# Kernel tuning notes

Hardware: AMD Instinct MI355X
Metric: run time of the kernel (lower is better)

The kernel has to match this reference:

```python
import jax, jax.numpy as jnp
import numpy as np

N = 20000
E = 320000
NEG_SLOPE = 0.2
LN_EPS = 1e-5


def gat_conv(x, W, a_src, a_dst, b, src, dst, heads, ch, concat):
    # x: [N, F_in]; W: [F_in, H*C]; a_src/a_dst: [H, C]; b: [H*C] or [C]
    xl = (x @ W).reshape(N, heads, ch)                      # [N,H,C]
    alpha_src = jnp.sum(xl * a_src, axis=-1)                # [N,H]
    alpha_dst = jnp.sum(xl * a_dst, axis=-1)                # [N,H]
    e = alpha_src[src] + alpha_dst[dst]                     # [E',H]
    e = jax.nn.leaky_relu(e, NEG_SLOPE)
    # segment softmax over incoming edges of each dst node
    m = jax.ops.segment_max(e, dst, num_segments=N)         # [N,H]
    m = jnp.where(jnp.isfinite(m), m, 0.0)
    ex = jnp.exp(e - m[dst])
    denom = jax.ops.segment_sum(ex, dst, num_segments=N)    # [N,H]
    alpha = ex / (denom[dst] + 1e-16)                       # [E',H]
    msg = alpha[:, :, None] * xl[src]                       # [E',H,C]
    out = jax.ops.segment_sum(msg, dst, num_segments=N)     # [N,H,C]
    if concat:
        return out.reshape(N, heads * ch) + b
    return out.mean(axis=1) + b


def layer_norm(x, g, b):
    mu = jnp.mean(x, axis=-1, keepdims=True)
    var = jnp.mean(jnp.square(x - mu), axis=-1, keepdims=True)
    return (x - mu) * jax.lax.rsqrt(var + LN_EPS) * g + b


def setup_inputs() -> dict:
    key = jax.random.key(0)
    ks = jax.random.split(key, 24)
    d = {}
    d["x"] = jax.random.normal(ks[0], (N, 50), dtype=jnp.float32)
    d["edge_index"] = jax.random.randint(ks[1], (2, E), 0, N, dtype=jnp.int64)

    def glorot(k, shape):
        fan = shape[0] + shape[-1]
        return jax.random.normal(k, shape, dtype=jnp.float32) * np.sqrt(2.0 / fan)

    # conv1: 50 -> 256, heads=4, concat
    d["W1"] = glorot(ks[2], (50, 4 * 256))
    d["a_src1"] = glorot(ks[3], (4, 256))
    d["a_dst1"] = glorot(ks[4], (4, 256))
    d["b1"] = jnp.zeros((4 * 256,), jnp.float32)
    # conv2: 1024 -> 256, heads=4, concat
    d["W2"] = glorot(ks[5], (1024, 4 * 256))
    d["a_src2"] = glorot(ks[6], (4, 256))
    d["a_dst2"] = glorot(ks[7], (4, 256))
    d["b2"] = jnp.zeros((4 * 256,), jnp.float32)
    # conv3: 1024 -> 121, heads=6, concat=False
    d["W3"] = glorot(ks[8], (1024, 6 * 121))
    d["a_src3"] = glorot(ks[9], (6, 121))
    d["a_dst3"] = glorot(ks[10], (6, 121))
    d["b3"] = jnp.zeros((121,), jnp.float32)
    # skips
    d["skipW1"] = glorot(ks[11], (50, 1024))
    d["skipb1"] = jnp.zeros((1024,), jnp.float32)
    d["skipW2"] = glorot(ks[12], (1024, 1024))
    d["skipb2"] = jnp.zeros((1024,), jnp.float32)
    # layer norms
    d["g1"] = jnp.ones((1024,), jnp.float32)
    d["beta1"] = jnp.zeros((1024,), jnp.float32)
    d["g2"] = jnp.ones((1024,), jnp.float32)
    d["beta2"] = jnp.zeros((1024,), jnp.float32)
    return d


def reference(x, edge_index, W1, a_src1, a_dst1, b1, W2, a_src2, a_dst2, b2,
              W3, a_src3, a_dst3, b3, skipW1, skipb1, skipW2, skipb2,
              g1, beta1, g2, beta2):
    # add self loops (PyG GATConv default)
    loop = jnp.arange(N, dtype=edge_index.dtype)
    src = jnp.concatenate([edge_index[0], loop])
    dst = jnp.concatenate([edge_index[1], loop])

    h = gat_conv(x, W1, a_src1, a_dst1, b1, src, dst, 4, 256, True)
    h = jax.nn.elu(layer_norm(h + (x @ skipW1 + skipb1), g1, beta1))
    h2 = gat_conv(h, W2, a_src2, a_dst2, b2, src, dst, 4, 256, True)
    h2 = jax.nn.elu(layer_norm(h2 + (h @ skipW2 + skipb2), g2, beta2))
    out = gat_conv(h2, W3, a_src3, a_dst3, b3, src, dst, 6, 121, False)
    return out
```

## Files before the change

kernel.cpp:

```cpp
#include <hip/hip_runtime.h>
#include <hip/hip_bf16.h>
#include <math.h>

typedef __attribute__((ext_vector_type(8))) __bf16 bf16x8;
typedef __attribute__((ext_vector_type(4))) float f32x4;

#if __has_builtin(__builtin_amdgcn_global_load_lds)
#define HAVE_GLD 1
#define GLD16(g, l)                                                                      \
    __builtin_amdgcn_global_load_lds(                                                    \
        (const __attribute__((address_space(1))) unsigned int*)(g),                      \
        (__attribute__((address_space(3))) unsigned int*)(l), 16, 0, 0)
#else
#define HAVE_GLD 0
#endif

__global__ __launch_bounds__(256) void gemm_bt(const __bf16* __restrict__ A,
                                               const __bf16* __restrict__ Bt,
                                               __bf16* __restrict__ C,
                                               int M, int N, int K) {
    __shared__ __bf16 As[128 * 32];
    __shared__ __bf16 Bs[128 * 32];
    const int t = threadIdx.x;
    const int lane = t & 63;
    const int wid = t >> 6;
    const int wm = (wid >> 1) << 6;
    const int wn = (wid & 1) << 6;
    const int bm = blockIdx.x * 128;
    const int bn = blockIdx.y * 128;

    const int srow = (wid << 4) + (lane >> 2);
    const int scol = (lane & 3) << 3;

    f32x4 acc[4][4];
#pragma unroll
    for (int i = 0; i < 4; i++)
#pragma unroll
        for (int j = 0; j < 4; j++) acc[i][j] = (f32x4){0.f, 0.f, 0.f, 0.f};

    const int m16 = lane & 15;
    const int k8 = (lane >> 4) << 3;

    for (int k0 = 0; k0 < K; k0 += 32) {
        __syncthreads();
#if HAVE_GLD
        GLD16(A + (size_t)(bm + srow) * K + k0 + scol, As + srow * 32 + scol);
        GLD16(A + (size_t)(bm + 64 + srow) * K + k0 + scol, As + (64 + srow) * 32 + scol);
        GLD16(Bt + (size_t)(bn + srow) * K + k0 + scol, Bs + srow * 32 + scol);
        GLD16(Bt + (size_t)(bn + 64 + srow) * K + k0 + scol, Bs + (64 + srow) * 32 + scol);
#else
        {
            bf16x8 a0 = *(const bf16x8*)(A + (size_t)(bm + srow) * K + k0 + scol);
            bf16x8 a1 = *(const bf16x8*)(A + (size_t)(bm + 64 + srow) * K + k0 + scol);
            bf16x8 b0 = *(const bf16x8*)(Bt + (size_t)(bn + srow) * K + k0 + scol);
            bf16x8 b1 = *(const bf16x8*)(Bt + (size_t)(bn + 64 + srow) * K + k0 + scol);
            *(bf16x8*)(As + srow * 32 + scol) = a0;
            *(bf16x8*)(As + (64 + srow) * 32 + scol) = a1;
            *(bf16x8*)(Bs + srow * 32 + scol) = b0;
            *(bf16x8*)(Bs + (64 + srow) * 32 + scol) = b1;
        }
#endif
        __syncthreads();
        bf16x8 af[4], bfr[4];
#pragma unroll
        for (int i = 0; i < 4; i++) {
            af[i] = *(const bf16x8*)(As + (wm + 16 * i + m16) * 32 + k8);
            bfr[i] = *(const bf16x8*)(Bs + (wn + 16 * i + m16) * 32 + k8);
        }
#pragma unroll
        for (int i = 0; i < 4; i++)
#pragma unroll
            for (int j = 0; j < 4; j++)
                acc[i][j] = __builtin_amdgcn_mfma_f32_16x16x32_bf16(af[i], bfr[j], acc[i][j], 0, 0, 0);
    }
    const int r4 = (lane >> 4) << 2;
#pragma unroll
    for (int i = 0; i < 4; i++) {
#pragma unroll
        for (int j = 0; j < 4; j++) {
            int col = bn + wn + 16 * j + m16;
#pragma unroll
            for (int r = 0; r < 4; r++) {
                int row = bm + wm + 16 * i + r4 + r;
                C[(size_t)row * N + col] = (__bf16)acc[i][j][r];
            }
        }
    }
}

__global__ void pack_x_k(const float* __restrict__ x, __bf16* __restrict__ xp, int rows_real) {
    int i = blockIdx.x * 256 + threadIdx.x;
    int n = i >> 6, c = i & 63;
    float v = 0.f;
    if (n < rows_real && c < 50) v = x[n * 50 + c];
    xp[(size_t)n * 64 + c] = (__bf16)v;
}

__global__ void transpose_pad_k(const float* __restrict__ W, __bf16* __restrict__ WT,
                                int K, int N, int Kp, int Np) {
    __shared__ float tile[32][33];
    int bx = blockIdx.x, by = blockIdx.y;
    int tx = threadIdx.x & 31, ty = threadIdx.x >> 5;
#pragma unroll
    for (int r = ty; r < 32; r += 8) {
        int k = by * 32 + r, n = bx * 32 + tx;
        float v = 0.f;
        if (k < K && n < N) v = W[(size_t)k * N + n];
        tile[r][tx] = v;
    }
    __syncthreads();
#pragma unroll
    for (int r = ty; r < 32; r += 8) {
        int n = bx * 32 + r, k = by * 32 + tx;
        if (n < Np && k < Kp) WT[(size_t)n * Kp + k] = (__bf16)tile[tx][r];
    }
}

__global__ void transpose_pad_w3_k(const float* __restrict__ W, __bf16* __restrict__ WT) {
    __shared__ float tile[32][33];
    int bx = blockIdx.x, by = blockIdx.y;
    int tx = threadIdx.x & 31, ty = threadIdx.x >> 5;
    int r0 = bx * 32;
    int h = r0 >> 7;
    int c0 = r0 & 127;
#pragma unroll
    for (int r = ty; r < 32; r += 8) {
        int k = by * 32 + r;
        int c = c0 + tx;
        float v = 0.f;
        if (c < 121) v = W[(size_t)k * 726 + h * 121 + c];
        tile[r][tx] = v;
    }
    __syncthreads();
#pragma unroll
    for (int r = ty; r < 32; r += 8) {
        int rr = r0 + r;
        int k = by * 32 + tx;
        WT[(size_t)rr * 1024 + k] = (__bf16)tile[tx][r];
    }
}

__global__ void probe_ei_k(const int* __restrict__ ei, int* __restrict__ flag) {
    if (blockIdx.x == 0 && threadIdx.x == 0) {
        int all0 = 1;
        for (int i = 0; i < 64; i++)
            if (ei[2 * i + 1] != 0) { all0 = 0; break; }
        *flag = all0;
    }
}

__device__ __forceinline__ int load_ei(const int* ei, int idx, int is64) {
    return is64 ? ei[2 * idx] : ei[idx];
}

__global__ void hist_k(const int* __restrict__ ei, const int* __restrict__ flag,
                       int* __restrict__ cnt, int E, int Nn) {
    int e = blockIdx.x * 256 + threadIdx.x;
    if (e >= E + Nn) return;
    int is64 = *flag;
    int d = (e < E) ? load_ei(ei, E + e, is64) : (e - E);
    d = min(max(d, 0), Nn - 1);
    atomicAdd(&cnt[d], 1);
}

__global__ __launch_bounds__(1024) void scan_k(const int* __restrict__ cnt, int* __restrict__ row_ptr,
                                               int Nn, int total) {
    __shared__ int part[1024];
    int t = threadIdx.x;
    int chunk = (Nn + 1023) >> 10;
    int lo = t * chunk;
    int hi = lo + chunk; if (hi > Nn) hi = Nn; if (lo > Nn) lo = Nn;
    int s = 0;
    for (int i = lo; i < hi; i++) s += cnt[i];
    part[t] = s;
    __syncthreads();
    for (int off = 1; off < 1024; off <<= 1) {
        int v = (t >= off) ? part[t - off] : 0;
        __syncthreads();
        part[t] += v;
        __syncthreads();
    }
    int run = part[t] - s;
    for (int i = lo; i < hi; i++) { row_ptr[i] = run; run += cnt[i]; }
    if (t == 0) row_ptr[Nn] = total;
}

__global__ void fill_csr_k(const int* __restrict__ ei, const int* __restrict__ flag,
                           const int* __restrict__ row_ptr, int* __restrict__ cursor,
                           int* __restrict__ src_csr, int E, int Nn) {
    int e = blockIdx.x * 256 + threadIdx.x;
    if (e >= E + Nn) return;
    int is64 = *flag;
    int d = (e < E) ? load_ei(ei, E + e, is64) : (e - E);
    int s = (e < E) ? load_ei(ei, e, is64) : (e - E);
    d = min(max(d, 0), Nn - 1);
    s = min(max(s, 0), Nn - 1);
    int slot = row_ptr[d] + atomicAdd(&cursor[d], 1);
    src_csr[slot] = s;
}

__global__ void alpha_k(const __bf16* __restrict__ XL, int ld, const float* __restrict__ a_src,
                        const float* __restrict__ a_dst, float* __restrict__ asrc,
                        float* __restrict__ adst, int Nn, int H, int C, int Cpad) {
    int gw = (blockIdx.x * 256 + threadIdx.x) >> 6;
    int lane = threadIdx.x & 63;
    if (gw >= Nn * H) return;
    int n = gw / H, h = gw - n * H;
    const __bf16* row = XL + (size_t)n * ld + h * Cpad;
    const float* as = a_src + h * C;
    const float* ad = a_dst + h * C;
    float s = 0.f, d = 0.f;
    for (int c = lane; c < C; c += 64) {
        float v = (float)row[c];
        s += v * as[c];
        d += v * ad[c];
    }
#pragma unroll
    for (int off = 32; off; off >>= 1) {
        s += __shfl_down(s, off);
        d += __shfl_down(d, off);
    }
    if (lane == 0) { asrc[n * H + h] = s; adst[n * H + h] = d; }
}

__global__ void attn_k(const int* __restrict__ row_ptr, const int* __restrict__ src_csr,
                       const float* __restrict__ asrc, const float* __restrict__ adst,
                       float* __restrict__ w, int Nn, int H) {
    int gw = (blockIdx.x * 256 + threadIdx.x) >> 6;
    int lane = threadIdx.x & 63;
    if (gw >= Nn) return;
    int n = gw;
    int base = row_ptr[n], deg = row_ptr[n + 1] - base;
    for (int h = 0; h < H; h++) {
        float ad = adst[n * H + h];
        float m = -1e30f;
        for (int s = lane; s < deg; s += 64) {
            float e = asrc[src_csr[base + s] * H + h] + ad;
            e = e > 0.f ? e : 0.2f * e;
            m = fmaxf(m, e);
        }
#pragma unroll
        for (int off = 1; off < 64; off <<= 1) m = fmaxf(m, __shfl_xor(m, off));
        float sum = 0.f;
        for (int s = lane; s < deg; s += 64) {
            float e = asrc[src_csr[base + s] * H + h] + ad;
            e = e > 0.f ? e : 0.2f * e;
            sum += __expf(e - m);
        }
#pragma unroll
        for (int off = 1; off < 64; off <<= 1) sum += __shfl_xor(sum, off);
        float inv = 1.f / (sum + 1e-16f);
        for (int s = lane; s < deg; s += 64) {
            float e = asrc[src_csr[base + s] * H + h] + ad;
            e = e > 0.f ? e : 0.2f * e;
            w[(size_t)(base + s) * H + h] = __expf(e - m) * inv;
        }
    }
}

__global__ __launch_bounds__(256) void agg_skip5(const __bf16* __restrict__ XL,
                                                 const float* __restrict__ w,
                                                 const int* __restrict__ row_ptr,
                                                 const int* __restrict__ src_csr,
                                                 const float* __restrict__ bias,
                                                 const float* __restrict__ sb,
                                                 __bf16* __restrict__ SK, int Nn) {
    const int cc = blockIdx.x;
    const int n = blockIdx.y * 4 + (threadIdx.x >> 6);
    const int lane = threadIdx.x & 63;
    if (n >= Nn) return;
    const int g = lane >> 4;
    const int p = lane & 15;
    const int col = cc * 128 + p * 8;
    const int head = cc >> 1;
    const int base = row_ptr[n], end = row_ptr[n + 1];

    float acc[8];
#pragma unroll
    for (int j = 0; j < 8; j++) acc[j] = 0.f;

    for (int e = base; e < end; e += 16) {
        int sidx[4];
        float wv[4];
#pragma unroll
        for (int s = 0; s < 4; s++) {
            int idx = e + g + 4 * s;
            bool v = idx < end;
            sidx[s] = v ? src_csr[idx] : src_csr[base];
            wv[s] = v ? w[(size_t)idx * 4 + head] : 0.f;
        }
#pragma unroll
        for (int s = 0; s < 4; s++) {
            bf16x8 xv = *(const bf16x8*)(XL + (size_t)sidx[s] * 1024 + col);
#pragma unroll
            for (int j = 0; j < 8; j++) acc[j] += wv[s] * (float)xv[j];
        }
    }
#pragma unroll
    for (int j = 0; j < 8; j++) {
        acc[j] += __shfl_xor(acc[j], 16);
        acc[j] += __shfl_xor(acc[j], 32);
    }
    if (lane < 16) {
        size_t o = (size_t)n * 1024 + col;
        bf16x8 sk = *(const bf16x8*)(SK + o);
        bf16x8 res;
#pragma unroll
        for (int j = 0; j < 8; j++)
            res[j] = (__bf16)(acc[j] + bias[col + j] + sb[col + j] + (float)sk[j]);
        *(bf16x8*)(SK + o) = res;
    }
}

__global__ __launch_bounds__(256) void agg_mean5(const __bf16* __restrict__ XL,
                                                 const float* __restrict__ w,
                                                 const int* __restrict__ row_ptr,
                                                 const int* __restrict__ src_csr,
                                                 __bf16* __restrict__ part, int Nn) {
    const int cc = blockIdx.x;
    const int n = blockIdx.y * 4 + (threadIdx.x >> 6);
    const int lane = threadIdx.x & 63;
    if (n >= Nn) return;
    const int g = lane >> 4;
    const int p = lane & 15;
    const int col = cc * 128 + p * 8;
    const int base = row_ptr[n], end = row_ptr[n + 1];

    float acc[8];
#pragma unroll
    for (int j = 0; j < 8; j++) acc[j] = 0.f;

    for (int e = base; e < end; e += 16) {
        int sidx[4];
        float wv[4];
#pragma unroll
        for (int s = 0; s < 4; s++) {
            int idx = e + g + 4 * s;
            bool v = idx < end;
            sidx[s] = v ? src_csr[idx] : src_csr[base];
            wv[s] = v ? w[(size_t)idx * 6 + cc] : 0.f;
        }
#pragma unroll
        for (int s = 0; s < 4; s++) {
            bf16x8 xv = *(const bf16x8*)(XL + (size_t)sidx[s] * 768 + col);
#pragma unroll
            for (int j = 0; j < 8; j++) acc[j] += wv[s] * (float)xv[j];
        }
    }
#pragma unroll
    for (int j = 0; j < 8; j++) {
        acc[j] += __shfl_xor(acc[j], 16);
        acc[j] += __shfl_xor(acc[j], 32);
    }
    if (lane < 16) {
        size_t o = (size_t)n * 768 + col;
        bf16x8 res;
#pragma unroll
        for (int j = 0; j < 8; j++) res[j] = (__bf16)acc[j];
        *(bf16x8*)(part + o) = res;
    }
}

__global__ __launch_bounds__(128) void reduce_mean_k(const __bf16* __restrict__ part,
                                                     const float* __restrict__ b3,
                                                     float* __restrict__ out, int Nn) {
    int n = blockIdx.x;
    int t = threadIdx.x;
    if (t >= 121) return;
    const __bf16* row = part + (size_t)n * 768;
    float s = 0.f;
#pragma unroll
    for (int h = 0; h < 6; h++) s += (float)row[h * 128 + t];
    out[(size_t)n * 121 + t] = s * (1.f / 6.f) + b3[t];
}

__global__ __launch_bounds__(256) void ln_elu_k(const __bf16* __restrict__ in,
                                                const float* __restrict__ g,
                                                const float* __restrict__ be,
                                                __bf16* __restrict__ out, int rows_real) {
    const int D = 1024;
    int n = blockIdx.x;
    int t = threadIdx.x;
    size_t ro = (size_t)n * D;
    if (n >= rows_real) {
#pragma unroll
        for (int j = 0; j < 4; j++) out[ro + t + 256 * j] = (__bf16)0.f;
        return;
    }
    float v[4];
    float s = 0.f, q = 0.f;
#pragma unroll
    for (int j = 0; j < 4; j++) {
        int c = t + 256 * j;
        float a = (float)in[ro + c];
        v[j] = a;
        s += a;
        q += a * a;
    }
#pragma unroll
    for (int off = 32; off; off >>= 1) {
        s += __shfl_down(s, off);
        q += __shfl_down(q, off);
    }
    __shared__ float rs[8];
    int wid = t >> 6;
    if ((t & 63) == 0) { rs[wid] = s; rs[wid + 4] = q; }
    __syncthreads();
    s = rs[0] + rs[1] + rs[2] + rs[3];
    q = rs[4] + rs[5] + rs[6] + rs[7];
    float mu = s * (1.f / 1024.f);
    float var = q * (1.f / 1024.f) - mu * mu;
    float inv = rsqrtf(fmaxf(var, 0.f) + 1e-5f);
#pragma unroll
    for (int j = 0; j < 4; j++) {
        int c = t + 256 * j;
        float y = (v[j] - mu) * inv * g[c] + be[c];
        y = y > 0.f ? y : expm1f(y);
        out[ro + c] = (__bf16)y;
    }
}

extern "C" void kernel_launch(void* const* d_in, const int* in_sizes, int n_in,
                              void* d_out, int out_size, void* d_ws, size_t ws_size,
                              hipStream_t stream) {
    const float* x   = (const float*)d_in[0];
    const int*   ei  = (const int*)d_in[1];
    const float* W1  = (const float*)d_in[2];
    const float* as1 = (const float*)d_in[3];
    const float* ad1 = (const float*)d_in[4];
    const float* b1  = (const float*)d_in[5];
    const float* W2  = (const float*)d_in[6];
    const float* as2 = (const float*)d_in[7];
    const float* ad2 = (const float*)d_in[8];
    const float* b2  = (const float*)d_in[9];
    const float* W3  = (const float*)d_in[10];
    const float* as3 = (const float*)d_in[11];
    const float* ad3 = (const float*)d_in[12];
    const float* b3  = (const float*)d_in[13];
    const float* sW1 = (const float*)d_in[14];
    const float* sb1 = (const float*)d_in[15];
    const float* sW2 = (const float*)d_in[16];
    const float* sb2 = (const float*)d_in[17];
    const float* g1  = (const float*)d_in[18];
    const float* be1 = (const float*)d_in[19];
    const float* g2  = (const float*)d_in[20];
    const float* be2 = (const float*)d_in[21];
    float* out = (float*)d_out;

    const int Nn = 20000;
    const int E = in_sizes[1] / 2;
    const int E2 = E + Nn;
    const int Mpad = 20096;

    char* p = (char*)d_ws;
    auto alloc = [&](size_t bytes) {
        char* r = p;
        p += (bytes + 255) & ~(size_t)255;
        return r;
    };
    __bf16* W1pT  = (__bf16*)alloc((size_t)1024 * 64 * 2);
    __bf16* sW1T  = (__bf16*)alloc((size_t)1024 * 64 * 2);
    __bf16* W2T   = (__bf16*)alloc((size_t)1024 * 1024 * 2);
    __bf16* sW2T  = (__bf16*)alloc((size_t)1024 * 1024 * 2);
    __bf16* W3pT  = (__bf16*)alloc((size_t)768 * 1024 * 2);
    __bf16* xp    = (__bf16*)alloc((size_t)Mpad * 64 * 2);
    __bf16* XL    = (__bf16*)alloc((size_t)Mpad * 1024 * 2);
    __bf16* SK    = (__bf16*)alloc((size_t)Mpad * 1024 * 2);
    __bf16* H1    = (__bf16*)alloc((size_t)Mpad * 1024 * 2);
    float*  asrcb = (float*)alloc((size_t)Nn * 6 * 4);
    float*  adstb = (float*)alloc((size_t)Nn * 6 * 4);
    float*  wbuf  = (float*)alloc((size_t)E2 * 6 * 4);
    int*    rowp  = (int*)alloc((size_t)(Nn + 1) * 4);
    int*    cnt   = (int*)alloc((size_t)Nn * 4);
    int*    scsr  = (int*)alloc((size_t)E2 * 4);
    int*    eiflag= (int*)alloc(256);
    __bf16* part  = SK;
    (void)ws_size; (void)n_in; (void)out_size;

    pack_x_k<<<(Mpad * 64) / 256, 256, 0, stream>>>(x, xp, Nn);
    transpose_pad_k<<<dim3(32, 2), 256, 0, stream>>>(W1, W1pT, 50, 1024, 64, 1024);
    transpose_pad_k<<<dim3(32, 2), 256, 0, stream>>>(sW1, sW1T, 50, 1024, 64, 1024);
    transpose_pad_k<<<dim3(32, 32), 256, 0, stream>>>(W2, W2T, 1024, 1024, 1024, 1024);
    transpose_pad_k<<<dim3(32, 32), 256, 0, stream>>>(sW2, sW2T, 1024, 1024, 1024, 1024);
    transpose_pad_w3_k<<<dim3(24, 32), 256, 0, stream>>>(W3, W3pT);

    probe_ei_k<<<1, 64, 0, stream>>>(ei, eiflag);
    hipMemsetAsync(cnt, 0, (size_t)Nn * 4, stream);
    hist_k<<<(E2 + 255) / 256, 256, 0, stream>>>(ei, eiflag, cnt, E, Nn);
    scan_k<<<1, 1024, 0, stream>>>(cnt, rowp, Nn, E2);
    hipMemsetAsync(cnt, 0, (size_t)Nn * 4, stream);
    fill_csr_k<<<(E2 + 255) / 256, 256, 0, stream>>>(ei, eiflag, rowp, cnt, scsr, E, Nn);

    gemm_bt<<<dim3(Mpad / 128, 8), 256, 0, stream>>>(xp, W1pT, XL, Mpad, 1024, 64);
    gemm_bt<<<dim3(Mpad / 128, 8), 256, 0, stream>>>(xp, sW1T, SK, Mpad, 1024, 64);
    alpha_k<<<(Nn * 4 * 64) / 256, 256, 0, stream>>>(XL, 1024, as1, ad1, asrcb, adstb, Nn, 4, 256, 256);
    attn_k<<<(Nn + 3) / 4, 256, 0, stream>>>(rowp, scsr, asrcb, adstb, wbuf, Nn, 4);
    agg_skip5<<<dim3(8, (Nn + 3) / 4), 256, 0, stream>>>(XL, wbuf, rowp, scsr, b1, sb1, SK, Nn);
    ln_elu_k<<<Mpad, 256, 0, stream>>>(SK, g1, be1, H1, Nn);

    gemm_bt<<<dim3(Mpad / 128, 8), 256, 0, stream>>>(H1, W2T, XL, Mpad, 1024, 1024);
    gemm_bt<<<dim3(Mpad / 128, 8), 256, 0, stream>>>(H1, sW2T, SK, Mpad, 1024, 1024);
    alpha_k<<<(Nn * 4 * 64) / 256, 256, 0, stream>>>(XL, 1024, as2, ad2, asrcb, adstb, Nn, 4, 256, 256);
    attn_k<<<(Nn + 3) / 4, 256, 0, stream>>>(rowp, scsr, asrcb, adstb, wbuf, Nn, 4);
    agg_skip5<<<dim3(8, (Nn + 3) / 4), 256, 0, stream>>>(XL, wbuf, rowp, scsr, b2, sb2, SK, Nn);
    ln_elu_k<<<Mpad, 256, 0, stream>>>(SK, g2, be2, H1, Nn);

    gemm_bt<<<dim3(Mpad / 128, 6), 256, 0, stream>>>(H1, W3pT, XL, Mpad, 768, 1024);
    alpha_k<<<(Nn * 6 * 64) / 256, 256, 0, stream>>>(XL, 768, as3, ad3, asrcb, adstb, Nn, 6, 121, 128);
    attn_k<<<(Nn + 3) / 4, 256, 0, stream>>>(rowp, scsr, asrcb, adstb, wbuf, Nn, 6);
    agg_mean5<<<dim3(6, (Nn + 3) / 4), 256, 0, stream>>>(XL, wbuf, rowp, scsr, part, Nn);
    reduce_mean_k<<<Nn, 128, 0, stream>>>(part, b3, out, Nn);
}
```

Before: 851.2 us.

## Pad CSR rows to 16 and store attention weights head-major for vector loads

Each node's CSR segment is rounded up to a multiple of 16 and zero-filled, and attention weights are stored as separate per-head planes. The aggregation kernels can then load source indices and weights as 16-byte vectors without bounds checks or the strided per-head weight gather. The cost is extra memsets of the enlarged CSR and weight buffers, padded zero-weight edges that still gather row 0 of XL, and a separate degree array (the fill cursor) to keep the true counts.

```diff
diff --git a/kernel.cpp b/kernel.cpp
--- a/kernel.cpp
+++ b/kernel.cpp
@@ -4,6 +4,7 @@
 
 typedef __attribute__((ext_vector_type(8))) __bf16 bf16x8;
 typedef __attribute__((ext_vector_type(4))) float f32x4;
+typedef __attribute__((ext_vector_type(4))) int i32x4;
 
 #if __has_builtin(__builtin_amdgcn_global_load_lds)
 #define HAVE_GLD 1
@@ -164,14 +165,14 @@
 }
 
 __global__ __launch_bounds__(1024) void scan_k(const int* __restrict__ cnt, int* __restrict__ row_ptr,
-                                               int Nn, int total) {
+                                               int Nn) {
     __shared__ int part[1024];
     int t = threadIdx.x;
     int chunk = (Nn + 1023) >> 10;
     int lo = t * chunk;
     int hi = lo + chunk; if (hi > Nn) hi = Nn; if (lo > Nn) lo = Nn;
     int s = 0;
-    for (int i = lo; i < hi; i++) s += cnt[i];
+    for (int i = lo; i < hi; i++) s += (cnt[i] + 15) & ~15;
     part[t] = s;
     __syncthreads();
     for (int off = 1; off < 1024; off <<= 1) {
@@ -181,8 +182,8 @@
         __syncthreads();
     }
     int run = part[t] - s;
-    for (int i = lo; i < hi; i++) { row_ptr[i] = run; run += cnt[i]; }
-    if (t == 0) row_ptr[Nn] = total;
+    for (int i = lo; i < hi; i++) { row_ptr[i] = run; run += (cnt[i] + 15) & ~15; }
+    if (t == 1023) row_ptr[Nn] = part[1023];
 }
 
 __global__ void fill_csr_k(const int* __restrict__ ei, const int* __restrict__ flag,
@@ -223,18 +224,19 @@
     if (lane == 0) { asrc[n * H + h] = s; adst[n * H + h] = d; }
 }
 
-__global__ void attn_k(const int* __restrict__ row_ptr, const int* __restrict__ src_csr,
+__global__ void attn_k(const int* __restrict__ row_ptr, const int* __restrict__ deg,
+                       const int* __restrict__ src_csr,
                        const float* __restrict__ asrc, const float* __restrict__ adst,
-                       float* __restrict__ w, int Nn, int H) {
+                       float* __restrict__ wt, int Nn, int H, int Epad) {
     int gw = (blockIdx.x * 256 + threadIdx.x) >> 6;
     int lane = threadIdx.x & 63;
     if (gw >= Nn) return;
     int n = gw;
-    int base = row_ptr[n], deg = row_ptr[n + 1] - base;
+    int base = row_ptr[n], dg = deg[n];
     for (int h = 0; h < H; h++) {
         float ad = adst[n * H + h];
         float m = -1e30f;
-        for (int s = lane; s < deg; s += 64) {
+        for (int s = lane; s < dg; s += 64) {
             float e = asrc[src_csr[base + s] * H + h] + ad;
             e = e > 0.f ? e : 0.2f * e;
             m = fmaxf(m, e);
@@ -242,7 +244,7 @@
 #pragma unroll
         for (int off = 1; off < 64; off <<= 1) m = fmaxf(m, __shfl_xor(m, off));
         float sum = 0.f;
-        for (int s = lane; s < deg; s += 64) {
+        for (int s = lane; s < dg; s += 64) {
             float e = asrc[src_csr[base + s] * H + h] + ad;
             e = e > 0.f ? e : 0.2f * e;
             sum += __expf(e - m);
@@ -250,21 +252,22 @@
 #pragma unroll
         for (int off = 1; off < 64; off <<= 1) sum += __shfl_xor(sum, off);
         float inv = 1.f / (sum + 1e-16f);
-        for (int s = lane; s < deg; s += 64) {
+        float* wrow = wt + (size_t)h * Epad;
+        for (int s = lane; s < dg; s += 64) {
             float e = asrc[src_csr[base + s] * H + h] + ad;
             e = e > 0.f ? e : 0.2f * e;
-            w[(size_t)(base + s) * H + h] = __expf(e - m) * inv;
-        }
-    }
-}
-
-__global__ __launch_bounds__(256) void agg_skip5(const __bf16* __restrict__ XL,
-                                                 const float* __restrict__ w,
+            wrow[base + s] = __expf(e - m) * inv;
+        }
+    }
+}
+
+__global__ __launch_bounds__(256) void agg_skip6(const __bf16* __restrict__ XL,
+                                                 const float* __restrict__ wt,
                                                  const int* __restrict__ row_ptr,
                                                  const int* __restrict__ src_csr,
                                                  const float* __restrict__ bias,
                                                  const float* __restrict__ sb,
-                                                 __bf16* __restrict__ SK, int Nn) {
+                                                 __bf16* __restrict__ SK, int Nn, int Epad) {
     const int cc = blockIdx.x;
     const int n = blockIdx.y * 4 + (threadIdx.x >> 6);
     const int lane = threadIdx.x & 63;
@@ -272,7 +275,8 @@
     const int g = lane >> 4;
     const int p = lane & 15;
     const int col = cc * 128 + p * 8;
-    const int head = cc >> 1;
+    const float* wrow = wt + (size_t)(cc >> 1) * Epad;
+    const __bf16* XLc = XL + col;
     const int base = row_ptr[n], end = row_ptr[n + 1];
 
     float acc[8];
@@ -280,18 +284,11 @@
     for (int j = 0; j < 8; j++) acc[j] = 0.f;
 
     for (int e = base; e < end; e += 16) {
-        int sidx[4];
-        float wv[4];
+        i32x4 si = *(const i32x4*)(src_csr + e + 4 * g);
+        f32x4 wv = *(const f32x4*)(wrow + e + 4 * g);
 #pragma unroll
         for (int s = 0; s < 4; s++) {
-            int idx = e + g + 4 * s;
-            bool v = idx < end;
-            sidx[s] = v ? src_csr[idx] : src_csr[base];
-            wv[s] = v ? w[(size_t)idx * 4 + head] : 0.f;
-        }
-#pragma unroll
-        for (int s = 0; s < 4; s++) {
-            bf16x8 xv = *(const bf16x8*)(XL + (size_t)sidx[s] * 1024 + col);
+            bf16x8 xv = *(const bf16x8*)(XLc + (size_t)si[s] * 1024);
 #pragma unroll
             for (int j = 0; j < 8; j++) acc[j] += wv[s] * (float)xv[j];
         }
@@ -312,11 +309,11 @@
     }
 }
 
-__global__ __launch_bounds__(256) void agg_mean5(const __bf16* __restrict__ XL,
-                                                 const float* __restrict__ w,
+__global__ __launch_bounds__(256) void agg_mean6(const __bf16* __restrict__ XL,
+                                                 const float* __restrict__ wt,
                                                  const int* __restrict__ row_ptr,
                                                  const int* __restrict__ src_csr,
-                                                 __bf16* __restrict__ part, int Nn) {
+                                                 __bf16* __restrict__ part, int Nn, int Epad) {
     const int cc = blockIdx.x;
     const int n = blockIdx.y * 4 + (threadIdx.x >> 6);
     const int lane = threadIdx.x & 63;
@@ -324,6 +321,8 @@
     const int g = lane >> 4;
     const int p = lane & 15;
     const int col = cc * 128 + p * 8;
+    const float* wrow = wt + (size_t)cc * Epad;
+    const __bf16* XLc = XL + col;
     const int base = row_ptr[n], end = row_ptr[n + 1];
 
     float acc[8];
@@ -331,18 +330,11 @@
     for (int j = 0; j < 8; j++) acc[j] = 0.f;
 
     for (int e = base; e < end; e += 16) {
-        int sidx[4];
-        float wv[4];
+        i32x4 si = *(const i32x4*)(src_csr + e + 4 * g);
+        f32x4 wv = *(const f32x4*)(wrow + e + 4 * g);
 #pragma unroll
         for (int s = 0; s < 4; s++) {
-            int idx = e + g + 4 * s;
-            bool v = idx < end;
-            sidx[s] = v ? src_csr[idx] : src_csr[base];
-            wv[s] = v ? w[(size_t)idx * 6 + cc] : 0.f;
-        }
-#pragma unroll
-        for (int s = 0; s < 4; s++) {
-            bf16x8 xv = *(const bf16x8*)(XL + (size_t)sidx[s] * 768 + col);
+            bf16x8 xv = *(const bf16x8*)(XLc + (size_t)si[s] * 768);
 #pragma unroll
             for (int j = 0; j < 8; j++) acc[j] += wv[s] * (float)xv[j];
         }
@@ -450,6 +442,7 @@
     const int Nn = 20000;
     const int E = in_sizes[1] / 2;
     const int E2 = E + Nn;
+    const int Ecap = E2 + 16 * Nn;
     const int Mpad = 20096;
 
     char* p = (char*)d_ws;
@@ -469,10 +462,10 @@
     __bf16* H1    = (__bf16*)alloc((size_t)Mpad * 1024 * 2);
     float*  asrcb = (float*)alloc((size_t)Nn * 6 * 4);
     float*  adstb = (float*)alloc((size_t)Nn * 6 * 4);
-    float*  wbuf  = (float*)alloc((size_t)E2 * 6 * 4);
+    float*  wbuf  = (float*)alloc((size_t)6 * Ecap * 4);
     int*    rowp  = (int*)alloc((size_t)(Nn + 1) * 4);
     int*    cnt   = (int*)alloc((size_t)Nn * 4);
-    int*    scsr  = (int*)alloc((size_t)E2 * 4);
+    int*    scsr  = (int*)alloc((size_t)Ecap * 4);
     int*    eiflag= (int*)alloc(256);
     __bf16* part  = SK;
     (void)ws_size; (void)n_in; (void)out_size;
@@ -487,27 +480,29 @@
     probe_ei_k<<<1, 64, 0, stream>>>(ei, eiflag);
     hipMemsetAsync(cnt, 0, (size_t)Nn * 4, stream);
     hist_k<<<(E2 + 255) / 256, 256, 0, stream>>>(ei, eiflag, cnt, E, Nn);
-    scan_k<<<1, 1024, 0, stream>>>(cnt, rowp, Nn, E2);
+    scan_k<<<1, 1024, 0, stream>>>(cnt, rowp, Nn);
     hipMemsetAsync(cnt, 0, (size_t)Nn * 4, stream);
+    hipMemsetAsync(scsr, 0, (size_t)Ecap * 4, stream);
+    hipMemsetAsync(wbuf, 0, (size_t)6 * Ecap * 4, stream);
     fill_csr_k<<<(E2 + 255) / 256, 256, 0, stream>>>(ei, eiflag, rowp, cnt, scsr, E, Nn);
 
     gemm_bt<<<dim3(Mpad / 128, 8), 256, 0, stream>>>(xp, W1pT, XL, Mpad, 1024, 64);
     gemm_bt<<<dim3(Mpad / 128, 8), 256, 0, stream>>>(xp, sW1T, SK, Mpad, 1024, 64);
     alpha_k<<<(Nn * 4 * 64) / 256, 256, 0, stream>>>(XL, 1024, as1, ad1, asrcb, adstb, Nn, 4, 256, 256);
-    attn_k<<<(Nn + 3) / 4, 256, 0, stream>>>(rowp, scsr, asrcb, adstb, wbuf, Nn, 4);
-    agg_skip5<<<dim3(8, (Nn + 3) / 4), 256, 0, stream>>>(XL, wbuf, rowp, scsr, b1, sb1, SK, Nn);
+    attn_k<<<(Nn + 3) / 4, 256, 0, stream>>>(rowp, cnt, scsr, asrcb, adstb, wbuf, Nn, 4, Ecap);
+    agg_skip6<<<dim3(8, (Nn + 3) / 4), 256, 0, stream>>>(XL, wbuf, rowp, scsr, b1, sb1, SK, Nn, Ecap);
     ln_elu_k<<<Mpad, 256, 0, stream>>>(SK, g1, be1, H1, Nn);
 
     gemm_bt<<<dim3(Mpad / 128, 8), 256, 0, stream>>>(H1, W2T, XL, Mpad, 1024, 1024);
     gemm_bt<<<dim3(Mpad / 128, 8), 256, 0, stream>>>(H1, sW2T, SK, Mpad, 1024, 1024);
     alpha_k<<<(Nn * 4 * 64) / 256, 256, 0, stream>>>(XL, 1024, as2, ad2, asrcb, adstb, Nn, 4, 256, 256);
-    attn_k<<<(Nn + 3) / 4, 256, 0, stream>>>(rowp, scsr, asrcb, adstb, wbuf, Nn, 4);
-    agg_skip5<<<dim3(8, (Nn + 3) / 4), 256, 0, stream>>>(XL, wbuf, rowp, scsr, b2, sb2, SK, Nn);
+    attn_k<<<(Nn + 3) / 4, 256, 0, stream>>>(rowp, cnt, scsr, asrcb, adstb, wbuf, Nn, 4, Ecap);
+    agg_skip6<<<dim3(8, (Nn + 3) / 4), 256, 0, stream>>>(XL, wbuf, rowp, scsr, b2, sb2, SK, Nn, Ecap);
     ln_elu_k<<<Mpad, 256, 0, stream>>>(SK, g2, be2, H1, Nn);
 
     gemm_bt<<<dim3(Mpad / 128, 6), 256, 0, stream>>>(H1, W3pT, XL, Mpad, 768, 1024);
     alpha_k<<<(Nn * 6 * 64) / 256, 256, 0, stream>>>(XL, 768, as3, ad3, asrcb, adstb, Nn, 6, 121, 128);
-    attn_k<<<(Nn + 3) / 4, 256, 0, stream>>>(rowp, scsr, asrcb, adstb, wbuf, Nn, 6);
-    agg_mean5<<<dim3(6, (Nn + 3) / 4), 256, 0, stream>>>(XL, wbuf, rowp, scsr, part, Nn);
+    attn_k<<<(Nn + 3) / 4, 256, 0, stream>>>(rowp, cnt, scsr, asrcb, adstb, wbuf, Nn, 6, Ecap);
+    agg_mean6<<<dim3(6, (Nn + 3) / 4), 256, 0, stream>>>(XL, wbuf, rowp, scsr, part, Nn, Ecap);
     reduce_mean_k<<<Nn, 128, 0, stream>>>(part, b3, out, Nn);
 }
```

After: 839.5 us. About the same (-1.4%).
